# Kernel optimization log

Measured on AMD Instinct MI355X. Metric: run time of the kernel, lower is better.

Reference implementation:

```python
import jax, jax.numpy as jnp
import numpy as np

E = 8          # num_experts
TOP_K = 2      # router top-k
ALPHA = 1.702  # swigluoai alpha
LIMIT = 7.0    # swigluoai clamp limit


def setup_inputs() -> dict:
    key = jax.random.key(0)
    ks = jax.random.split(key, 7)
    B, S, H, I = 2, 1024, 1024, 1024
    s = 1.0 / np.sqrt(H)  # keep activations O(1), realistic init scale
    return {
        "x": jax.random.normal(ks[0], (B, S, H), jnp.float32),
        "router_weight": jax.random.normal(ks[1], (E, H), jnp.float32) * s,
        "router_bias": jax.random.normal(ks[2], (E,), jnp.float32) * 0.01,
        "w1": jax.random.normal(ks[3], (E, H, 2 * I), jnp.float32) * s,  # interleaved gate/up
        "w1_bias": jax.random.normal(ks[4], (E, 2 * I), jnp.float32) * 0.01,
        "w2": jax.random.normal(ks[5], (E, I, H), jnp.float32) * s,
        "w2_bias": jax.random.normal(ks[6], (E, H), jnp.float32) * 0.01,
    }


def _moe(x, router_weight, router_bias, w1, w1_bias, w2, w2_bias):
    B, S, H = x.shape
    xf = x.reshape(-1, H)                                   # [T, H]
    # ---- router: softmax over expert logits, then top-k ----
    logits = xf @ router_weight.T + router_bias             # [T, E]
    probs = jax.nn.softmax(logits, axis=-1)
    expert_weights, expert_ids = jax.lax.top_k(probs, TOP_K)  # [T, k]
    # combine weights scattered to dense [T, E] (no normalization: normalize_expert_weights=None)
    combine = jnp.sum(jax.nn.one_hot(expert_ids, E, dtype=xf.dtype)
                      * expert_weights[..., None], axis=1)  # [T, E]
    # ---- grouped MLP, expressed densely per expert (reference semantics) ----
    h = jnp.einsum('th,ehi->eti', xf, w1) + w1_bias[:, None, :]   # [E, T, 2I]
    gate = h[..., 0::2]                                          # interleaved layout
    up = h[..., 1::2]
    gate = jnp.minimum(gate, LIMIT)                              # swigluoai: clamp gate max
    up = jnp.clip(up, -LIMIT, LIMIT)                             # clamp up both sides
    glu = gate * jax.nn.sigmoid(gate * ALPHA)
    act = (up + 1.0) * glu                                       # [E, T, I]
    y = jnp.einsum('eti,eih->eth', act, w2) + w2_bias[:, None, :]  # [E, T, H]
    out = jnp.einsum('eth,te->th', y, combine)                   # weighted combine
    return out.reshape(B, S, H), expert_weights


def reference(x, router_weight, router_bias, w1, w1_bias, w2, w2_bias):
    return _moe(x, router_weight, router_bias, w1, w1_bias, w2, w2_bias)
```

## Files before the change

kernel.cpp:

```cpp
#include <hip/hip_runtime.h>
#include <cstdint>
#include <cstddef>

typedef unsigned short u16;
typedef short bf16x8 __attribute__((ext_vector_type(8)));
typedef float floatx4 __attribute__((ext_vector_type(4)));

#define GLD16(gp, sp) __builtin_amdgcn_global_load_lds(                      \
    (const __attribute__((address_space(1))) void*)(gp),                     \
    (__attribute__((address_space(3))) void*)(sp), 16, 0, 0)

__device__ __forceinline__ u16 f2bf(float f) {
  unsigned u = __float_as_uint(f);
  u += 0x7fffu + ((u >> 16) & 1u);
  return (u16)(u >> 16);
}

__global__ __launch_bounds__(256) void prep_kernel(
    const float* __restrict__ x, const float* __restrict__ rw, const float* __restrict__ rbias,
    const float* __restrict__ w1, const float* __restrict__ w2,
    u16* __restrict__ xb, u16* __restrict__ w1t, u16* __restrict__ w2t,
    float* __restrict__ ew, int* __restrict__ eids, float* __restrict__ eprobs) {
  __shared__ float lds[64 * 33];
  const int b = blockIdx.x, tid = threadIdx.x;
  if (b < 1024) {
    const float4* in4 = (const float4*)x;
    ushort4* out4 = (ushort4*)xb;
    int i = (b << 8) + tid;
#pragma unroll
    for (int rep = 0; rep < 2; ++rep, i += 262144) {
      float4 v = in4[i];
      ushort4 o;
      o.x = f2bf(v.x); o.y = f2bf(v.y); o.z = f2bf(v.z); o.w = f2bf(v.w);
      out4[i] = o;
    }
  } else if (b < 13312) {
    const float* in; u16* out; int C, r0, c0;
    if (b < 9216) {
      int b2 = b - 1024, e = b2 >> 10, rem = b2 & 1023;
      C = 2048; r0 = (rem >> 6) << 6; c0 = (rem & 63) << 5;
      in = w1 + (size_t)e * 2097152; out = w1t + (size_t)e * 2097152;
    } else {
      int b2 = b - 9216, e = b2 >> 9, rem = b2 & 511;
      C = 1024; r0 = (rem >> 5) << 6; c0 = (rem & 31) << 5;
      in = w2 + (size_t)e * 1048576; out = w2t + (size_t)e * 1048576;
    }
    const int tx = tid & 31, ty = tid >> 5;
#pragma unroll
    for (int k = 0; k < 8; ++k) {
      int row = k * 8 + ty;
      lds[row * 33 + tx] = in[(size_t)(r0 + row) * C + c0 + tx];
    }
    __syncthreads();
#pragma unroll
    for (int k = 0; k < 4; ++k) {
      int cc = k * 8 + ty;
      ushort2 v;
      v.x = f2bf(lds[(tx * 2) * 33 + cc]);
      v.y = f2bf(lds[(tx * 2 + 1) * 33 + cc]);
      *(ushort2*)(out + (size_t)(c0 + cc) * 1024 + r0 + tx * 2) = v;
    }
  } else {
    const int wave = tid >> 6, lane = tid & 63;
    const int t = ((b - 13312) << 2) + wave;
    const float4* xv = (const float4*)(x + (size_t)t * 1024);
    float acc[8];
#pragma unroll
    for (int e = 0; e < 8; ++e) acc[e] = 0.f;
    for (int j = lane; j < 256; j += 64) {
      float4 xx = xv[j];
#pragma unroll
      for (int e = 0; e < 8; ++e) {
        float4 wv = ((const float4*)(rw + (size_t)e * 1024))[j];
        acc[e] += xx.x * wv.x + xx.y * wv.y + xx.z * wv.z + xx.w * wv.w;
      }
    }
#pragma unroll
    for (int e = 0; e < 8; ++e) {
      float v = acc[e];
#pragma unroll
      for (int off = 32; off > 0; off >>= 1) v += __shfl_down(v, off);
      acc[e] = v;
    }
    if (lane == 0) {
      float p[8];
      float mx = -1e30f;
#pragma unroll
      for (int e = 0; e < 8; ++e) { p[e] = acc[e] + rbias[e]; mx = fmaxf(mx, p[e]); }
      float sum = 0.f;
#pragma unroll
      for (int e = 0; e < 8; ++e) { p[e] = __expf(p[e] - mx); sum += p[e]; }
      float inv = 1.f / sum;
#pragma unroll
      for (int e = 0; e < 8; ++e) p[e] *= inv;
      int i0 = 0;
#pragma unroll
      for (int e = 1; e < 8; ++e) if (p[e] > p[i0]) i0 = e;
      int i1 = (i0 == 0) ? 1 : 0;
#pragma unroll
      for (int e = 0; e < 8; ++e) if (e != i0 && e != i1 && p[e] > p[i1]) i1 = e;
      ew[t * 2 + 0] = p[i0];
      ew[t * 2 + 1] = p[i1];
      eids[t * 2 + 0] = i0;
      eids[t * 2 + 1] = i1;
      eprobs[t * 2 + 0] = p[i0];
      eprobs[t * 2 + 1] = p[i1];
    }
  }
}

__global__ void build_lists_kernel(const int* __restrict__ eids, const float* __restrict__ eprobs,
                                   int* __restrict__ row_token, float* __restrict__ row_scale,
                                   int* __restrict__ meta) {
  __shared__ int cnt[8], base[8], cur[8];
  const int tid = threadIdx.x;
  if (tid < 8) { cnt[tid] = 0; cur[tid] = 0; }
  __syncthreads();
  for (int t = tid; t < 2048; t += 256) {
    atomicAdd(&cnt[eids[t * 2 + 0]], 1);
    atomicAdd(&cnt[eids[t * 2 + 1]], 1);
  }
  __syncthreads();
  if (tid == 0) {
    int off = 0, w = 0;
    for (int e = 0; e < 8; ++e) {
      base[e] = off;
      meta[48 + e] = off;
      int nb = (cnt[e] + 127) >> 7;
      for (int rb = 0; rb < nb; ++rb) meta[1 + w++] = (e << 8) | rb;
      off += nb << 7;
    }
    meta[0] = w;
  }
  __syncthreads();
  for (int s = tid; s < 5120; s += 256) { row_token[s] = -1; row_scale[s] = 0.f; }
  __syncthreads();
  for (int t = tid; t < 2048; t += 256) {
#pragma unroll
    for (int k = 0; k < 2; ++k) {
      int e = eids[t * 2 + k];
      int s = base[e] + atomicAdd(&cur[e], 1);
      row_token[s] = t;
      row_scale[s] = eprobs[t * 2 + k];
    }
  }
}

__global__ void bias_init_kernel(const int* __restrict__ eids, const float* __restrict__ eprobs,
                                 const float* __restrict__ w2b, float* __restrict__ out) {
  int idx = blockIdx.x * 256 + threadIdx.x;
  int t = idx >> 8, h4 = idx & 255;
  const float4* b4 = (const float4*)w2b;
  float4 v0 = b4[eids[2 * t] * 256 + h4];
  float4 v1 = b4[eids[2 * t + 1] * 256 + h4];
  float p0 = eprobs[2 * t], p1 = eprobs[2 * t + 1];
  float4 r;
  r.x = p0 * v0.x + p1 * v1.x;
  r.y = p0 * v0.y + p1 * v1.y;
  r.z = p0 * v0.z + p1 * v1.z;
  r.w = p0 * v0.w + p1 * v1.w;
  ((float4*)out)[idx] = r;
}

__global__ __launch_bounds__(256) void gemm1_act_kernel(
    const u16* __restrict__ xb, const u16* __restrict__ w1t,
    const float* __restrict__ w1b,
    const int* __restrict__ row_token, const float* __restrict__ row_scale,
    const int* __restrict__ meta, u16* __restrict__ actS) {
  const int d = blockIdx.x;
  const int xcd = d & 7, i = d >> 3;
  const int work = i >> 2;
  if (work >= meta[0]) return;
  const int colBase = (xcd + ((i & 3) << 3)) << 6;
  const int wk = meta[1 + work];
  const int e = wk >> 8, rb = wk & 255;
  const int slotB = meta[48 + e] + (rb << 7);
  __shared__ __align__(16) u16 As[4096];
  __shared__ __align__(16) u16 Bs[2048];
  const int tid = threadIdx.x, lane = tid & 63, wave = tid >> 6;
  const int row16 = lane & 15, chunk = lane >> 4;
  const u16* Bt = w1t + (size_t)e * 2097152;
  int tk0 = row_token[slotB + wave * 16 + row16];       if (tk0 < 0) tk0 = 0;
  int tk1 = row_token[slotB + (wave + 4) * 16 + row16]; if (tk1 < 0) tk1 = 0;
  const u16* aP0 = xb + (size_t)tk0 * 1024 + chunk * 8;
  const u16* aP1 = xb + (size_t)tk1 * 1024 + chunk * 8;
  const u16* bP  = Bt + (size_t)(colBase + wave * 16 + row16) * 1024 + chunk * 8;
  const int wr = wave >> 1, wc = wave & 1;
  floatx4 acc[4][2];
#pragma unroll
  for (int mi = 0; mi < 4; ++mi)
#pragma unroll
    for (int ni = 0; ni < 2; ++ni) acc[mi][ni] = floatx4{0.f, 0.f, 0.f, 0.f};

  for (int kt = 0; kt < 32; ++kt) {
    const int k = kt * 32;
    GLD16(aP0 + k, As + wave * 512);
    GLD16(aP1 + k, As + (4 + wave) * 512);
    GLD16(bP + k, Bs + wave * 512);
    __syncthreads();
    bf16x8 af[4], bfr[2];
#pragma unroll
    for (int mi = 0; mi < 4; ++mi) af[mi] = *(const bf16x8*)(As + (wr * 4 + mi) * 512 + lane * 8);
#pragma unroll
    for (int ni = 0; ni < 2; ++ni) bfr[ni] = *(const bf16x8*)(Bs + (wc * 2 + ni) * 512 + lane * 8);
#pragma unroll
    for (int mi = 0; mi < 4; ++mi)
#pragma unroll
      for (int ni = 0; ni < 2; ++ni)
        acc[mi][ni] = __builtin_amdgcn_mfma_f32_16x16x32_bf16(af[mi], bfr[ni], acc[mi][ni], 0, 0, 0);
    __syncthreads();
  }

  const int cl = lane & 15, ql = lane >> 4;
#pragma unroll
  for (int mi = 0; mi < 4; ++mi) {
#pragma unroll
    for (int r = 0; r < 4; ++r) {
      const int slot = slotB + wr * 64 + mi * 16 + ql * 4 + r;
      const float c = row_scale[slot];
#pragma unroll
      for (int ni = 0; ni < 2; ++ni) {
        const int n = colBase + wc * 32 + ni * 16 + cl;
        float v = acc[mi][ni][r] + w1b[e * 2048 + n];
        float o = __shfl_xor(v, 1);
        if ((lane & 1) == 0) {
          float g = fminf(v, 7.f);
          float u = fminf(fmaxf(o, -7.f), 7.f);
          float sg = 1.f / (1.f + __expf(-1.702f * g));
          float a = (u + 1.f) * (g * sg);
          actS[(size_t)slot * 1024 + (n >> 1)] = f2bf(c * a);
        }
      }
    }
  }
}

__global__ __launch_bounds__(256) void gemm2_add_kernel(
    const u16* __restrict__ actS, const u16* __restrict__ w2t,
    const int* __restrict__ row_token, const int* __restrict__ meta,
    float* __restrict__ out) {
  const int d = blockIdx.x;
  const int xcd = d & 7, i = d >> 3;
  const int j = i >> 1;
  const int ks = (j >= 40) ? 1 : 0;
  const int work = j - ks * 40;
  if (work >= meta[0]) return;
  const int colBase = (xcd + ((i & 1) << 3)) << 6;
  const int k0 = ks << 9;
  const int wk = meta[1 + work];
  const int e = wk >> 8, rb = wk & 255;
  const int slotB = meta[48 + e] + (rb << 7);
  __shared__ __align__(16) u16 As[4096];
  __shared__ __align__(16) u16 Bs[2048];
  const int tid = threadIdx.x, lane = tid & 63, wave = tid >> 6;
  const int row16 = lane & 15, chunk = lane >> 4;
  const u16* Bt = w2t + (size_t)e * 1048576;
  const u16* aP0 = actS + (size_t)(slotB + wave * 16 + row16) * 1024 + chunk * 8;
  const u16* aP1 = actS + (size_t)(slotB + (wave + 4) * 16 + row16) * 1024 + chunk * 8;
  const u16* bP  = Bt + (size_t)(colBase + wave * 16 + row16) * 1024 + chunk * 8;
  const int wr = wave >> 1, wc = wave & 1;
  floatx4 acc[4][2];
#pragma unroll
  for (int mi = 0; mi < 4; ++mi)
#pragma unroll
    for (int ni = 0; ni < 2; ++ni) acc[mi][ni] = floatx4{0.f, 0.f, 0.f, 0.f};

  for (int kt = 0; kt < 16; ++kt) {
    const int k = k0 + kt * 32;
    GLD16(aP0 + k, As + wave * 512);
    GLD16(aP1 + k, As + (4 + wave) * 512);
    GLD16(bP + k, Bs + wave * 512);
    __syncthreads();
    bf16x8 af[4], bfr[2];
#pragma unroll
    for (int mi = 0; mi < 4; ++mi) af[mi] = *(const bf16x8*)(As + (wr * 4 + mi) * 512 + lane * 8);
#pragma unroll
    for (int ni = 0; ni < 2; ++ni) bfr[ni] = *(const bf16x8*)(Bs + (wc * 2 + ni) * 512 + lane * 8);
#pragma unroll
    for (int mi = 0; mi < 4; ++mi)
#pragma unroll
      for (int ni = 0; ni < 2; ++ni)
        acc[mi][ni] = __builtin_amdgcn_mfma_f32_16x16x32_bf16(af[mi], bfr[ni], acc[mi][ni], 0, 0, 0);
    __syncthreads();
  }

  const int cl = lane & 15, ql = lane >> 4;
#pragma unroll
  for (int mi = 0; mi < 4; ++mi)
#pragma unroll
    for (int r = 0; r < 4; ++r) {
      const int slot = slotB + wr * 64 + mi * 16 + ql * 4 + r;
      const int tok = row_token[slot];
      if (tok < 0) continue;
#pragma unroll
      for (int ni = 0; ni < 2; ++ni) {
        const int col = colBase + wc * 32 + ni * 16 + cl;
        atomicAdd(out + (size_t)tok * 1024 + col, acc[mi][ni][r]);
      }
    }
}

extern "C" void kernel_launch(void* const* d_in, const int* in_sizes, int n_in,
                              void* d_out, int out_size, void* d_ws, size_t ws_size,
                              hipStream_t stream) {
  const float* x   = (const float*)d_in[0];
  const float* rw  = (const float*)d_in[1];
  const float* rb  = (const float*)d_in[2];
  const float* w1  = (const float*)d_in[3];
  const float* w1b = (const float*)d_in[4];
  const float* w2  = (const float*)d_in[5];
  const float* w2b = (const float*)d_in[6];
  float* out = (float*)d_out;
  float* ew  = out + (size_t)2048 * 1024;

  char* ws = (char*)d_ws;
  u16* xb        = (u16*)(ws);
  u16* w1t       = (u16*)(ws + (4ull << 20));
  u16* w2t       = (u16*)(ws + (36ull << 20));
  u16* actS      = (u16*)(ws + (52ull << 20));
  int* eids      = (int*)(ws + (62ull << 20));
  float* eprobs  = (float*)(ws + (62ull << 20) + (16 << 10));
  int* row_token = (int*)(ws + (62ull << 20) + (32 << 10));
  float* row_scale = (float*)(ws + (62ull << 20) + (52 << 10));
  int* meta      = (int*)(ws + (62ull << 20) + (72 << 10));

  prep_kernel<<<13824, 256, 0, stream>>>(x, rw, rb, w1, w2, xb, w1t, w2t, ew, eids, eprobs);
  build_lists_kernel<<<1, 256, 0, stream>>>(eids, eprobs, row_token, row_scale, meta);
  bias_init_kernel<<<2048, 256, 0, stream>>>(eids, eprobs, w2b, out);
  gemm1_act_kernel<<<1280, 256, 0, stream>>>(xb, w1t, w1b, row_token, row_scale, meta, actS);
  gemm2_add_kernel<<<1280, 256, 0, stream>>>(actS, w2t, row_token, meta, out);
}
```

Before: 274.2 us.

## Fuse routing list build into prep, widen GEMM tiles, fold bias into GEMM2

Expert slot lists are now built with global atomics inside the router part of prep_kernel, using fixed 2048-slot segments per expert. This removes the separate build_lists and bias_init kernels and replaces them with memsets. The w2 bias, scaled by the routing probability, is added in the first K-split of GEMM2 instead of in a separate pass. Both GEMMs move from 128x64 to 128x128 tiles with a K step of 64, giving more MFMA work per LDS load and barrier. The cost is a larger grid with many early-exit blocks, plus nondeterministic slot order and padded rows that write zeros to token 0.

```diff
diff --git a/kernel.cpp b/kernel.cpp
--- a/kernel.cpp
+++ b/kernel.cpp
@@ -20,7 +20,8 @@
     const float* __restrict__ x, const float* __restrict__ rw, const float* __restrict__ rbias,
     const float* __restrict__ w1, const float* __restrict__ w2,
     u16* __restrict__ xb, u16* __restrict__ w1t, u16* __restrict__ w2t,
-    float* __restrict__ ew, int* __restrict__ eids, float* __restrict__ eprobs) {
+    float* __restrict__ ew, int* __restrict__ row_token, float* __restrict__ row_scale,
+    int* __restrict__ cnt) {
   __shared__ float lds[64 * 33];
   const int b = blockIdx.x, tid = threadIdx.x;
   if (b < 1024) {
@@ -101,113 +102,72 @@
       for (int e = 0; e < 8; ++e) if (e != i0 && e != i1 && p[e] > p[i1]) i1 = e;
       ew[t * 2 + 0] = p[i0];
       ew[t * 2 + 1] = p[i1];
-      eids[t * 2 + 0] = i0;
-      eids[t * 2 + 1] = i1;
-      eprobs[t * 2 + 0] = p[i0];
-      eprobs[t * 2 + 1] = p[i1];
+      int s0 = atomicAdd(&cnt[i0], 1);
+      row_token[(i0 << 11) + s0] = t;
+      row_scale[(i0 << 11) + s0] = p[i0];
+      int s1 = atomicAdd(&cnt[i1], 1);
+      row_token[(i1 << 11) + s1] = t;
+      row_scale[(i1 << 11) + s1] = p[i1];
     }
   }
-}
-
-__global__ void build_lists_kernel(const int* __restrict__ eids, const float* __restrict__ eprobs,
-                                   int* __restrict__ row_token, float* __restrict__ row_scale,
-                                   int* __restrict__ meta) {
-  __shared__ int cnt[8], base[8], cur[8];
-  const int tid = threadIdx.x;
-  if (tid < 8) { cnt[tid] = 0; cur[tid] = 0; }
-  __syncthreads();
-  for (int t = tid; t < 2048; t += 256) {
-    atomicAdd(&cnt[eids[t * 2 + 0]], 1);
-    atomicAdd(&cnt[eids[t * 2 + 1]], 1);
-  }
-  __syncthreads();
-  if (tid == 0) {
-    int off = 0, w = 0;
-    for (int e = 0; e < 8; ++e) {
-      base[e] = off;
-      meta[48 + e] = off;
-      int nb = (cnt[e] + 127) >> 7;
-      for (int rb = 0; rb < nb; ++rb) meta[1 + w++] = (e << 8) | rb;
-      off += nb << 7;
-    }
-    meta[0] = w;
-  }
-  __syncthreads();
-  for (int s = tid; s < 5120; s += 256) { row_token[s] = -1; row_scale[s] = 0.f; }
-  __syncthreads();
-  for (int t = tid; t < 2048; t += 256) {
-#pragma unroll
-    for (int k = 0; k < 2; ++k) {
-      int e = eids[t * 2 + k];
-      int s = base[e] + atomicAdd(&cur[e], 1);
-      row_token[s] = t;
-      row_scale[s] = eprobs[t * 2 + k];
-    }
-  }
-}
-
-__global__ void bias_init_kernel(const int* __restrict__ eids, const float* __restrict__ eprobs,
-                                 const float* __restrict__ w2b, float* __restrict__ out) {
-  int idx = blockIdx.x * 256 + threadIdx.x;
-  int t = idx >> 8, h4 = idx & 255;
-  const float4* b4 = (const float4*)w2b;
-  float4 v0 = b4[eids[2 * t] * 256 + h4];
-  float4 v1 = b4[eids[2 * t + 1] * 256 + h4];
-  float p0 = eprobs[2 * t], p1 = eprobs[2 * t + 1];
-  float4 r;
-  r.x = p0 * v0.x + p1 * v1.x;
-  r.y = p0 * v0.y + p1 * v1.y;
-  r.z = p0 * v0.z + p1 * v1.z;
-  r.w = p0 * v0.w + p1 * v1.w;
-  ((float4*)out)[idx] = r;
 }
 
 __global__ __launch_bounds__(256) void gemm1_act_kernel(
     const u16* __restrict__ xb, const u16* __restrict__ w1t,
     const float* __restrict__ w1b,
     const int* __restrict__ row_token, const float* __restrict__ row_scale,
-    const int* __restrict__ meta, u16* __restrict__ actS) {
+    const int* __restrict__ cnt, u16* __restrict__ actS) {
   const int d = blockIdx.x;
-  const int xcd = d & 7, i = d >> 3;
-  const int work = i >> 2;
-  if (work >= meta[0]) return;
-  const int colBase = (xcd + ((i & 3) << 3)) << 6;
-  const int wk = meta[1 + work];
-  const int e = wk >> 8, rb = wk & 255;
-  const int slotB = meta[48 + e] + (rb << 7);
-  __shared__ __align__(16) u16 As[4096];
-  __shared__ __align__(16) u16 Bs[2048];
+  const int xcd = d & 7, j = d >> 3;
+  const int colHi = j & 1, rb = (j >> 1) & 15, e = j >> 5;
+  if (rb * 128 >= cnt[e]) return;
+  const int colBase = (xcd + (colHi << 3)) << 7;
+  const int slotB = (e << 11) + (rb << 7);
+  __shared__ __align__(16) u16 As[128 * 64];
+  __shared__ __align__(16) u16 Bs[128 * 64];
   const int tid = threadIdx.x, lane = tid & 63, wave = tid >> 6;
   const int row16 = lane & 15, chunk = lane >> 4;
   const u16* Bt = w1t + (size_t)e * 2097152;
-  int tk0 = row_token[slotB + wave * 16 + row16];       if (tk0 < 0) tk0 = 0;
-  int tk1 = row_token[slotB + (wave + 4) * 16 + row16]; if (tk1 < 0) tk1 = 0;
+  const int g0 = wave * 2, g1 = wave * 2 + 1;
+  int tk0 = row_token[slotB + g0 * 16 + row16];
+  int tk1 = row_token[slotB + g1 * 16 + row16];
   const u16* aP0 = xb + (size_t)tk0 * 1024 + chunk * 8;
   const u16* aP1 = xb + (size_t)tk1 * 1024 + chunk * 8;
-  const u16* bP  = Bt + (size_t)(colBase + wave * 16 + row16) * 1024 + chunk * 8;
+  const u16* bP0 = Bt + (size_t)(colBase + g0 * 16 + row16) * 1024 + chunk * 8;
+  const u16* bP1 = Bt + (size_t)(colBase + g1 * 16 + row16) * 1024 + chunk * 8;
   const int wr = wave >> 1, wc = wave & 1;
-  floatx4 acc[4][2];
+  floatx4 acc[4][4];
 #pragma unroll
   for (int mi = 0; mi < 4; ++mi)
 #pragma unroll
-    for (int ni = 0; ni < 2; ++ni) acc[mi][ni] = floatx4{0.f, 0.f, 0.f, 0.f};
-
-  for (int kt = 0; kt < 32; ++kt) {
-    const int k = kt * 32;
-    GLD16(aP0 + k, As + wave * 512);
-    GLD16(aP1 + k, As + (4 + wave) * 512);
-    GLD16(bP + k, Bs + wave * 512);
-    __syncthreads();
-    bf16x8 af[4], bfr[2];
-#pragma unroll
-    for (int mi = 0; mi < 4; ++mi) af[mi] = *(const bf16x8*)(As + (wr * 4 + mi) * 512 + lane * 8);
-#pragma unroll
-    for (int ni = 0; ni < 2; ++ni) bfr[ni] = *(const bf16x8*)(Bs + (wc * 2 + ni) * 512 + lane * 8);
-#pragma unroll
-    for (int mi = 0; mi < 4; ++mi)
-#pragma unroll
-      for (int ni = 0; ni < 2; ++ni)
-        acc[mi][ni] = __builtin_amdgcn_mfma_f32_16x16x32_bf16(af[mi], bfr[ni], acc[mi][ni], 0, 0, 0);
+    for (int ni = 0; ni < 4; ++ni) acc[mi][ni] = floatx4{0.f, 0.f, 0.f, 0.f};
+
+  for (int kt = 0; kt < 16; ++kt) {
+    const int k = kt * 64;
+    GLD16(aP0 + k,      As + g0 * 1024);
+    GLD16(aP0 + k + 32, As + g0 * 1024 + 512);
+    GLD16(aP1 + k,      As + g1 * 1024);
+    GLD16(aP1 + k + 32, As + g1 * 1024 + 512);
+    GLD16(bP0 + k,      Bs + g0 * 1024);
+    GLD16(bP0 + k + 32, Bs + g0 * 1024 + 512);
+    GLD16(bP1 + k,      Bs + g1 * 1024);
+    GLD16(bP1 + k + 32, Bs + g1 * 1024 + 512);
+    __syncthreads();
+#pragma unroll
+    for (int kh = 0; kh < 2; ++kh) {
+      bf16x8 af[4], bfr[4];
+#pragma unroll
+      for (int mi = 0; mi < 4; ++mi)
+        af[mi] = *(const bf16x8*)(As + (wr * 4 + mi) * 1024 + kh * 512 + lane * 8);
+#pragma unroll
+      for (int ni = 0; ni < 4; ++ni)
+        bfr[ni] = *(const bf16x8*)(Bs + (wc * 4 + ni) * 1024 + kh * 512 + lane * 8);
+#pragma unroll
+      for (int mi = 0; mi < 4; ++mi)
+#pragma unroll
+        for (int ni = 0; ni < 4; ++ni)
+          acc[mi][ni] = __builtin_amdgcn_mfma_f32_16x16x32_bf16(af[mi], bfr[ni], acc[mi][ni], 0, 0, 0);
+    }
     __syncthreads();
   }
 
@@ -219,8 +179,8 @@
       const int slot = slotB + wr * 64 + mi * 16 + ql * 4 + r;
       const float c = row_scale[slot];
 #pragma unroll
-      for (int ni = 0; ni < 2; ++ni) {
-        const int n = colBase + wc * 32 + ni * 16 + cl;
+      for (int ni = 0; ni < 4; ++ni) {
+        const int n = colBase + wc * 64 + ni * 16 + cl;
         float v = acc[mi][ni][r] + w1b[e * 2048 + n];
         float o = __shfl_xor(v, 1);
         if ((lane & 1) == 0) {
@@ -236,51 +196,59 @@
 }
 
 __global__ __launch_bounds__(256) void gemm2_add_kernel(
-    const u16* __restrict__ actS, const u16* __restrict__ w2t,
-    const int* __restrict__ row_token, const int* __restrict__ meta,
-    float* __restrict__ out) {
+    const u16* __restrict__ actS, const u16* __restrict__ w2t, const float* __restrict__ w2b,
+    const int* __restrict__ row_token, const float* __restrict__ row_scale,
+    const int* __restrict__ cnt, float* __restrict__ out) {
   const int d = blockIdx.x;
-  const int xcd = d & 7, i = d >> 3;
-  const int j = i >> 1;
-  const int ks = (j >= 40) ? 1 : 0;
-  const int work = j - ks * 40;
-  if (work >= meta[0]) return;
-  const int colBase = (xcd + ((i & 1) << 3)) << 6;
+  const int xcd = d & 7, j = d >> 3;
+  const int ks = j & 1, rb = (j >> 1) & 15, e = j >> 5;
+  if (rb * 128 >= cnt[e]) return;
+  const int colBase = xcd << 7;
+  const int slotB = (e << 11) + (rb << 7);
   const int k0 = ks << 9;
-  const int wk = meta[1 + work];
-  const int e = wk >> 8, rb = wk & 255;
-  const int slotB = meta[48 + e] + (rb << 7);
-  __shared__ __align__(16) u16 As[4096];
-  __shared__ __align__(16) u16 Bs[2048];
+  __shared__ __align__(16) u16 As[128 * 64];
+  __shared__ __align__(16) u16 Bs[128 * 64];
   const int tid = threadIdx.x, lane = tid & 63, wave = tid >> 6;
   const int row16 = lane & 15, chunk = lane >> 4;
   const u16* Bt = w2t + (size_t)e * 1048576;
-  const u16* aP0 = actS + (size_t)(slotB + wave * 16 + row16) * 1024 + chunk * 8;
-  const u16* aP1 = actS + (size_t)(slotB + (wave + 4) * 16 + row16) * 1024 + chunk * 8;
-  const u16* bP  = Bt + (size_t)(colBase + wave * 16 + row16) * 1024 + chunk * 8;
+  const int g0 = wave * 2, g1 = wave * 2 + 1;
+  const u16* aP0 = actS + (size_t)(slotB + g0 * 16 + row16) * 1024 + chunk * 8;
+  const u16* aP1 = actS + (size_t)(slotB + g1 * 16 + row16) * 1024 + chunk * 8;
+  const u16* bP0 = Bt + (size_t)(colBase + g0 * 16 + row16) * 1024 + chunk * 8;
+  const u16* bP1 = Bt + (size_t)(colBase + g1 * 16 + row16) * 1024 + chunk * 8;
   const int wr = wave >> 1, wc = wave & 1;
-  floatx4 acc[4][2];
+  floatx4 acc[4][4];
 #pragma unroll
   for (int mi = 0; mi < 4; ++mi)
 #pragma unroll
-    for (int ni = 0; ni < 2; ++ni) acc[mi][ni] = floatx4{0.f, 0.f, 0.f, 0.f};
-
-  for (int kt = 0; kt < 16; ++kt) {
-    const int k = k0 + kt * 32;
-    GLD16(aP0 + k, As + wave * 512);
-    GLD16(aP1 + k, As + (4 + wave) * 512);
-    GLD16(bP + k, Bs + wave * 512);
-    __syncthreads();
-    bf16x8 af[4], bfr[2];
-#pragma unroll
-    for (int mi = 0; mi < 4; ++mi) af[mi] = *(const bf16x8*)(As + (wr * 4 + mi) * 512 + lane * 8);
-#pragma unroll
-    for (int ni = 0; ni < 2; ++ni) bfr[ni] = *(const bf16x8*)(Bs + (wc * 2 + ni) * 512 + lane * 8);
-#pragma unroll
-    for (int mi = 0; mi < 4; ++mi)
-#pragma unroll
-      for (int ni = 0; ni < 2; ++ni)
-        acc[mi][ni] = __builtin_amdgcn_mfma_f32_16x16x32_bf16(af[mi], bfr[ni], acc[mi][ni], 0, 0, 0);
+    for (int ni = 0; ni < 4; ++ni) acc[mi][ni] = floatx4{0.f, 0.f, 0.f, 0.f};
+
+  for (int kt = 0; kt < 8; ++kt) {
+    const int k = k0 + kt * 64;
+    GLD16(aP0 + k,      As + g0 * 1024);
+    GLD16(aP0 + k + 32, As + g0 * 1024 + 512);
+    GLD16(aP1 + k,      As + g1 * 1024);
+    GLD16(aP1 + k + 32, As + g1 * 1024 + 512);
+    GLD16(bP0 + k,      Bs + g0 * 1024);
+    GLD16(bP0 + k + 32, Bs + g0 * 1024 + 512);
+    GLD16(bP1 + k,      Bs + g1 * 1024);
+    GLD16(bP1 + k + 32, Bs + g1 * 1024 + 512);
+    __syncthreads();
+#pragma unroll
+    for (int kh = 0; kh < 2; ++kh) {
+      bf16x8 af[4], bfr[4];
+#pragma unroll
+      for (int mi = 0; mi < 4; ++mi)
+        af[mi] = *(const bf16x8*)(As + (wr * 4 + mi) * 1024 + kh * 512 + lane * 8);
+#pragma unroll
+      for (int ni = 0; ni < 4; ++ni)
+        bfr[ni] = *(const bf16x8*)(Bs + (wc * 4 + ni) * 1024 + kh * 512 + lane * 8);
+#pragma unroll
+      for (int mi = 0; mi < 4; ++mi)
+#pragma unroll
+        for (int ni = 0; ni < 4; ++ni)
+          acc[mi][ni] = __builtin_amdgcn_mfma_f32_16x16x32_bf16(af[mi], bfr[ni], acc[mi][ni], 0, 0, 0);
+    }
     __syncthreads();
   }
 
@@ -291,11 +259,13 @@
     for (int r = 0; r < 4; ++r) {
       const int slot = slotB + wr * 64 + mi * 16 + ql * 4 + r;
       const int tok = row_token[slot];
-      if (tok < 0) continue;
-#pragma unroll
-      for (int ni = 0; ni < 2; ++ni) {
-        const int col = colBase + wc * 32 + ni * 16 + cl;
-        atomicAdd(out + (size_t)tok * 1024 + col, acc[mi][ni][r]);
+      const float p = row_scale[slot];
+#pragma unroll
+      for (int ni = 0; ni < 4; ++ni) {
+        const int col = colBase + wc * 64 + ni * 16 + cl;
+        float v = acc[mi][ni][r];
+        if (ks == 0) v += p * w2b[e * 1024 + col];
+        atomicAdd(out + (size_t)tok * 1024 + col, v);
       }
     }
 }
@@ -318,15 +288,14 @@
   u16* w1t       = (u16*)(ws + (4ull << 20));
   u16* w2t       = (u16*)(ws + (36ull << 20));
   u16* actS      = (u16*)(ws + (52ull << 20));
-  int* eids      = (int*)(ws + (62ull << 20));
-  float* eprobs  = (float*)(ws + (62ull << 20) + (16 << 10));
-  int* row_token = (int*)(ws + (62ull << 20) + (32 << 10));
-  float* row_scale = (float*)(ws + (62ull << 20) + (52 << 10));
-  int* meta      = (int*)(ws + (62ull << 20) + (72 << 10));
-
-  prep_kernel<<<13824, 256, 0, stream>>>(x, rw, rb, w1, w2, xb, w1t, w2t, ew, eids, eprobs);
-  build_lists_kernel<<<1, 256, 0, stream>>>(eids, eprobs, row_token, row_scale, meta);
-  bias_init_kernel<<<2048, 256, 0, stream>>>(eids, eprobs, w2b, out);
-  gemm1_act_kernel<<<1280, 256, 0, stream>>>(xb, w1t, w1b, row_token, row_scale, meta, actS);
-  gemm2_add_kernel<<<1280, 256, 0, stream>>>(actS, w2t, row_token, meta, out);
-}
+  int* row_token = (int*)(ws + (84ull << 20));
+  float* row_scale = (float*)(ws + (84ull << 20) + (64 << 10));
+  int* cnt       = (int*)(ws + (84ull << 20) + (128 << 10));
+
+  hipMemsetAsync(out, 0, (size_t)2048 * 1024 * 4, stream);
+  hipMemsetAsync(row_token, 0, (128 << 10) + 32, stream);
+  prep_kernel<<<13824, 256, 0, stream>>>(x, rw, rb, w1, w2, xb, w1t, w2t,
+                                         ew, row_token, row_scale, cnt);
+  gemm1_act_kernel<<<2048, 256, 0, stream>>>(xb, w1t, w1b, row_token, row_scale, cnt, actS);
+  gemm2_add_kernel<<<2048, 256, 0, stream>>>(actS, w2t, w2b, row_token, row_scale, cnt, out);
+}
```

Result: slower. 396.2 us (+44.5%).
